# Kernel optimization log

Hardware: AMD Instinct MI355X
Metric: run time of the kernel (lower is better)

The kernel has to match this reference:

```python
import jax, jax.numpy as jnp
import numpy as np

B, H, W, C = 4, 64, 64, 256
D = C // 8  # reduction_ratio = 8


def setup_inputs() -> dict:
    key = jax.random.key(0)
    ks = jax.random.split(key, 6)
    scale = 1.0 / np.sqrt(C)
    return {
        "x": jax.random.normal(ks[0], (B, H, W, C), dtype=jnp.float32),
        "Wf": jax.random.normal(ks[1], (C, D), dtype=jnp.float32) * scale,
        "Wg": jax.random.normal(ks[2], (C, D), dtype=jnp.float32) * scale,
        "Wh": jax.random.normal(ks[3], (C, D), dtype=jnp.float32) * scale,
        "Wv": jax.random.normal(ks[4], (D, C), dtype=jnp.float32) * (1.0 / np.sqrt(D)),
        "gamma": jax.random.normal(ks[5], (), dtype=jnp.float32),
    }


def reference(x, Wf, Wg, Wh, Wv, gamma):
    b, h, w, c = x.shape
    n = h * w
    xf = x.reshape(b, n, c)
    # 1x1 convs (no bias) == per-pixel matmuls over channels
    q = xf @ Wf  # [b, n, d]
    k = xf @ Wg  # [b, n, d]
    v = xf @ Wh  # [b, n, d]
    # beta[i, j] = k_i . q_j ; softmax over last (query) axis, unscaled
    beta = jax.nn.softmax(jnp.einsum('bnd,bmd->bnm', k, q), axis=-1)  # [b, n, n]
    o = jnp.einsum('bnm,bmd->bnd', beta, v)  # [b, n, d]
    o = o.reshape(b, h, w, -1) @ Wv  # output 1x1 conv -> [b, h, w, c]
    return gamma * o + x
```

## Files before the change

### kernel.cpp

```cpp
#include <hip/hip_runtime.h>
#include <hip/hip_bf16.h>
#include <stdint.h>


typedef __attribute__((ext_vector_type(8))) short bf16x8;
typedef __attribute__((ext_vector_type(4))) short bf16x4;
typedef __attribute__((ext_vector_type(8))) _Float16 f16x8;
typedef __attribute__((ext_vector_type(4))) float f32x4;
typedef unsigned short ushort_t;

static __device__ __forceinline__ ushort_t f2bf(float f) {
    __hip_bfloat16 h = __float2bfloat16(f);
    return __builtin_bit_cast(ushort_t, h);
}
static __device__ __forceinline__ float bf2f(ushort_t u) {
    return __bfloat162float(__builtin_bit_cast(__hip_bfloat16, u));
}
static __device__ __forceinline__ ushort_t f2h(float f) {
    _Float16 h = (_Float16)f;
    return __builtin_bit_cast(ushort_t, h);
}
static __device__ __forceinline__ void tsplit(float w, ushort_t& hi, ushort_t& lo) {
    uint32_t b = __builtin_bit_cast(uint32_t, w);
    hi = (ushort_t)(b >> 16);
    float hf = __builtin_bit_cast(float, b & 0xFFFF0000u);
    lo = f2bf(w - hf);
}

static __device__ __forceinline__ f32x4 mfma16bf(bf16x4 a, bf16x4 b, f32x4 c) {
#if __has_builtin(__builtin_amdgcn_mfma_f32_16x16x16bf16_1k)
    return __builtin_amdgcn_mfma_f32_16x16x16bf16_1k(a, b, c, 0, 0, 0);
#else
    f32x4 d;
    asm("v_mfma_f32_16x16x16_bf16 %0, %1, %2, %3"
        : "=v"(d) : "v"(a), "v"(b), "v"(c));
    return d;
#endif
}

static __device__ __forceinline__ float fexp2(float x) {
#if __has_builtin(__builtin_amdgcn_exp2f)
    return __builtin_amdgcn_exp2f(x);
#else
    return exp2f(x);
#endif
}

#define NROWS 16384
#define NTOK  4096
#define QKS   40
#define LOG2E 1.44269504088896340736f

__global__ __launch_bounds__(256) void qkv_kernel(
    const float* __restrict__ x,
    const float* __restrict__ Wf, const float* __restrict__ Wg,
    const float* __restrict__ Wh,
    ushort_t* __restrict__ qh,
    ushort_t* __restrict__ kf,
    ushort_t* __restrict__ vT)
{
    __shared__ __align__(16) ushort_t xh[32 * QKS];
    __shared__ __align__(16) ushort_t xl[32 * QKS];

    const int tid  = threadIdx.x;
    const int wave = tid >> 6;
    const int lane = tid & 63;
    const int ln15 = lane & 15;
    const int quad = lane >> 4;
    const int row0 = blockIdx.x * 32;
    const int rg     = wave & 1;
    const int cgbase = wave >> 1;
    const int r  = tid >> 3;
    const int pp = (tid & 7) * 4;

    f32x4 acc[3];
    #pragma unroll
    for (int ci = 0; ci < 3; ++ci) acc[ci] = (f32x4){0.f, 0.f, 0.f, 0.f};

    float4 xa = *reinterpret_cast<const float4*>(&x[(row0 + r) * 256 + pp]);

    for (int k0 = 0; k0 < 256; k0 += 32) {
        bf16x8 bh[3], bl[3];
        #pragma unroll
        for (int ci = 0; ci < 3; ++ci) {
            int cg = cgbase + ci * 2;
            const float* Wsrc = (cg < 2) ? Wf : (cg < 4) ? Wg : Wh;
            int c = (cg & 1) * 16 + ln15;
            ushort_t hv8[8], lv8[8];
            #pragma unroll
            for (int j = 0; j < 8; ++j) {
                float w = Wsrc[(k0 + quad * 8 + j) * 32 + c];
                tsplit(w, hv8[j], lv8[j]);
            }
            bh[ci] = *reinterpret_cast<bf16x8*>(hv8);
            bl[ci] = *reinterpret_cast<bf16x8*>(lv8);
        }
        float fv[4];
        *reinterpret_cast<float4*>(fv) = xa;
        ushort_t hv[4], lv[4];
        #pragma unroll
        for (int j = 0; j < 4; ++j) tsplit(fv[j], hv[j], lv[j]);
        __syncthreads();
        *reinterpret_cast<uint2*>(&xh[r * QKS + pp]) = *reinterpret_cast<uint2*>(hv);
        *reinterpret_cast<uint2*>(&xl[r * QKS + pp]) = *reinterpret_cast<uint2*>(lv);
        __syncthreads();
        if (k0 < 224)
            xa = *reinterpret_cast<const float4*>(&x[(row0 + r) * 256 + k0 + 32 + pp]);

        const bf16x8 ah = *reinterpret_cast<const bf16x8*>(
            &xh[(rg * 16 + ln15) * QKS + quad * 8]);
        const bf16x8 al = *reinterpret_cast<const bf16x8*>(
            &xl[(rg * 16 + ln15) * QKS + quad * 8]);
        #pragma unroll
        for (int ci = 0; ci < 3; ++ci) {
            acc[ci] = __builtin_amdgcn_mfma_f32_16x16x32_bf16(ah, bh[ci], acc[ci], 0, 0, 0);
            acc[ci] = __builtin_amdgcn_mfma_f32_16x16x32_bf16(al, bh[ci], acc[ci], 0, 0, 0);
            acc[ci] = __builtin_amdgcn_mfma_f32_16x16x32_bf16(ah, bl[ci], acc[ci], 0, 0, 0);
        }
    }

    #pragma unroll
    for (int ci = 0; ci < 3; ++ci) {
        int cg = cgbase + ci * 2;
        int cc = (cg & 1) * 16 + ln15;
        int rowb = row0 + rg * 16 + quad * 4;
        if (cg < 2) {
            #pragma unroll
            for (int rr = 0; rr < 4; ++rr)
                qh[(rowb + rr) * 32 + cc] = f2h(acc[ci][rr] * LOG2E);
        } else if (cg < 4) {
            #pragma unroll
            for (int rr = 0; rr < 4; ++rr)
                kf[(rowb + rr) * 32 + cc] = f2h(acc[ci][rr]);
        } else {
            int bb = row0 >> 12;
            int m  = (row0 & 4095) + rg * 16 + quad * 4;
            ushort4 h4;
            h4.x = f2bf(acc[ci][0]);
            h4.y = f2bf(acc[ci][1]);
            h4.z = f2bf(acc[ci][2]);
            h4.w = f2bf(acc[ci][3]);
            *reinterpret_cast<ushort4*>(&vT[bb * 131072 + cc * 4096 + m]) = h4;
        }
    }
}

__global__ __launch_bounds__(1024, 4) void attn_kernel(
    const ushort_t* __restrict__ qhg,
    const ushort_t* __restrict__ kfg,
    const ushort_t* __restrict__ vT,
    const float* __restrict__ Wv, const float* __restrict__ x,
    const float* __restrict__ gamma, float* __restrict__ out)
{
    __shared__ float Ored[8][32][65];
    __shared__ float Lred[8][64];
    __shared__ float wv[8192];
    __shared__ float Os[64][33];
    __shared__ float linv[64];

    const int tid  = threadIdx.x;
    const int wave = tid >> 6;
    const int lane = tid & 63;
    const int ln15 = lane & 15;
    const int quad = lane >> 4;

    const int b    = blockIdx.x >> 6;
    const int n0   = (blockIdx.x & 63) * 64;
    const int base = b * NTOK;
    const int bb   = b * 131072;

    f16x8 khf[4];
    #pragma unroll
    for (int t = 0; t < 4; ++t)
        khf[t] = *reinterpret_cast<const f16x8*>(
            &kfg[(base + n0 + t * 16 + ln15) * 32 + quad * 8]);

    #pragma unroll
    for (int i = 0; i < 8; ++i) wv[tid + i * 1024] = Wv[tid + i * 1024];

    f32x4 accO[2][4];
    #pragma unroll
    for (int s01 = 0; s01 < 2; ++s01)
        #pragma unroll
        for (int t = 0; t < 4; ++t)
            accO[s01][t] = (f32x4){0.f, 0.f, 0.f, 0.f};
    float lacc[4] = {0.f, 0.f, 0.f, 0.f};

    const int mbase = wave * 16;
    const ushort_t* qp  = qhg + (size_t)(base + mbase + ln15) * 32 + quad * 8;
    const ushort_t* vp0 = vT + bb + ln15 * 4096 + mbase + quad * 4;
    const ushort_t* vp1 = vp0 + 16 * 4096;

    f16x8  qf  = *reinterpret_cast<const f16x8*>(qp);
    bf16x4 va0 = *reinterpret_cast<const bf16x4*>(vp0);
    bf16x4 va1 = *reinterpret_cast<const bf16x4*>(vp1);

    for (int it = 0; it < 16; ++it) {
        qp  += 256 * 32;
        vp0 += 256;
        vp1 += 256;
        f16x8  nqf  = *reinterpret_cast<const f16x8*>(qp);
        bf16x4 nva0 = *reinterpret_cast<const bf16x4*>(vp0);
        bf16x4 nva1 = *reinterpret_cast<const bf16x4*>(vp1);

        #pragma unroll
        for (int t = 0; t < 4; ++t) {
            f32x4 s = __builtin_amdgcn_mfma_f32_16x16x32_f16(
                qf, khf[t], (f32x4){0.f, 0.f, 0.f, 0.f}, 0, 0, 0);

            float p0 = fexp2(s[0]);
            float p1 = fexp2(s[1]);
            float p2 = fexp2(s[2]);
            float p3 = fexp2(s[3]);
            lacc[t] += (p0 + p1) + (p2 + p3);

            ushort_t pu[4];
            pu[0] = f2bf(p0);
            pu[1] = f2bf(p1);
            pu[2] = f2bf(p2);
            pu[3] = f2bf(p3);
            const bf16x4 pb = *reinterpret_cast<bf16x4*>(pu);

            accO[0][t] = mfma16bf(va0, pb, accO[0][t]);
            accO[1][t] = mfma16bf(va1, pb, accO[1][t]);
        }
        qf = nqf; va0 = nva0; va1 = nva1;
    }

    float lr[4];
    #pragma unroll
    for (int t = 0; t < 4; ++t) {
        float v = lacc[t];
        v += __shfl_xor(v, 16);
        v += __shfl_xor(v, 32);
        lr[t] = v;
    }
    if (wave < 8) {
        #pragma unroll
        for (int s01 = 0; s01 < 2; ++s01)
            #pragma unroll
            for (int t = 0; t < 4; ++t)
                #pragma unroll
                for (int rr = 0; rr < 4; ++rr)
                    Ored[wave][s01 * 16 + quad * 4 + rr][t * 16 + ln15] = accO[s01][t][rr];
        if (quad == 0) {
            #pragma unroll
            for (int t = 0; t < 4; ++t) Lred[wave][t * 16 + ln15] = lr[t];
        }
    }
    __syncthreads();
    if (wave >= 8) {
        const int ws = wave - 8;
        #pragma unroll
        for (int s01 = 0; s01 < 2; ++s01)
            #pragma unroll
            for (int t = 0; t < 4; ++t)
                #pragma unroll
                for (int rr = 0; rr < 4; ++rr)
                    Ored[ws][s01 * 16 + quad * 4 + rr][t * 16 + ln15] += accO[s01][t][rr];
        if (quad == 0) {
            #pragma unroll
            for (int t = 0; t < 4; ++t) Lred[ws][t * 16 + ln15] += lr[t];
        }
    }
    __syncthreads();

    #pragma unroll
    for (int i = 0; i < 2; ++i) {
        int idx = i * 1024 + tid;
        int d = idx & 31;
        int n = idx >> 5;
        float v = (Ored[0][d][n] + Ored[1][d][n]) + (Ored[2][d][n] + Ored[3][d][n])
                + (Ored[4][d][n] + Ored[5][d][n]) + (Ored[6][d][n] + Ored[7][d][n]);
        Os[n][d] = v;
    }
    if (tid < 64) {
        float s = (Lred[0][tid] + Lred[1][tid]) + (Lred[2][tid] + Lred[3][tid])
                + (Lred[4][tid] + Lred[5][tid]) + (Lred[6][tid] + Lred[7][tid]);
        linv[tid] = 1.0f / s;
    }
    __syncthreads();

    const float g  = gamma[0];
    const int   c  = tid & 255;
    const int   nh = (tid >> 8) * 16;
    const int rowb = base + n0 + nh;
    #pragma unroll
    for (int rc = 0; rc < 16; rc += 8) {
        float acc[8];
        #pragma unroll
        for (int rr = 0; rr < 8; ++rr) acc[rr] = 0.f;
        for (int d = 0; d < 32; ++d) {
            float wvd = wv[d * 256 + c];
            #pragma unroll
            for (int rr = 0; rr < 8; ++rr) acc[rr] += Os[nh + rc + rr][d] * wvd;
        }
        #pragma unroll
        for (int rr = 0; rr < 8; ++rr) {
            int row = rowb + rc + rr;
            out[row * 256 + c] = g * acc[rr] * linv[nh + rc + rr] + x[row * 256 + c];
        }
    }
}

extern "C" void kernel_launch(void* const* d_in, const int* in_sizes, int n_in,
                              void* d_out, int out_size, void* d_ws, size_t ws_size,
                              hipStream_t stream)
{
    const float* x     = (const float*)d_in[0];
    const float* Wf    = (const float*)d_in[1];
    const float* Wg    = (const float*)d_in[2];
    const float* Wh    = (const float*)d_in[3];
    const float* Wv    = (const float*)d_in[4];
    const float* gamma = (const float*)d_in[5];
    float* out = (float*)d_out;

    ushort_t* qh = (ushort_t*)d_ws;
    ushort_t* kf = qh + NROWS * 32;
    ushort_t* vT = kf + NROWS * 32;

    qkv_kernel<<<dim3(512), dim3(256), 0, stream>>>(x, Wf, Wg, Wh, qh, kf, vT);
    attn_kernel<<<dim3(256), dim3(1024), 0, stream>>>(qh, kf, vT, Wv, x, gamma, out);
}
```

Baseline: 112.8 us.

## Fuse QKV projection and attention into one cooperative kernel with grid sync

Merges the QKV projection kernel and the attention kernel into a single cooperative launch of 256 blocks of 1024 threads. Each block first computes 64 rows of Q/K/V, with the work re-split across 16 waves, then does a grid-wide sync before the attention phase. The Wv shared-memory load is moved ahead of the projection phase. This removes one kernel launch and its gap between kernels, at the cost of a grid barrier, a projection phase in which only half the threads load x, and reliance on all 256 blocks being co-resident.

```diff
diff --git a/kernel.cpp b/kernel.cpp
--- a/kernel.cpp
+++ b/kernel.cpp
@@ -1,7 +1,10 @@
 #include <hip/hip_runtime.h>
 #include <hip/hip_bf16.h>
+#include <hip/hip_cooperative_groups.h>
 #include <stdint.h>
 
+
+namespace cg = cooperative_groups;
 
 typedef __attribute__((ext_vector_type(8))) short bf16x8;
 typedef __attribute__((ext_vector_type(4))) short bf16x4;
@@ -51,118 +54,125 @@
 #define QKS   40
 #define LOG2E 1.44269504088896340736f
 
-__global__ __launch_bounds__(256) void qkv_kernel(
+__global__ __launch_bounds__(1024, 4) void fused_kernel(
     const float* __restrict__ x,
     const float* __restrict__ Wf, const float* __restrict__ Wg,
-    const float* __restrict__ Wh,
-    ushort_t* __restrict__ qh,
-    ushort_t* __restrict__ kf,
+    const float* __restrict__ Wh, const float* __restrict__ Wv,
+    const float* __restrict__ gamma, float* __restrict__ out,
+    ushort_t* __restrict__ qhg,
+    ushort_t* __restrict__ kfg,
     ushort_t* __restrict__ vT)
 {
-    __shared__ __align__(16) ushort_t xh[32 * QKS];
-    __shared__ __align__(16) ushort_t xl[32 * QKS];
+    __shared__ __align__(16) ushort_t xh[64 * QKS];
+    __shared__ __align__(16) ushort_t xl[64 * QKS];
+    __shared__ float Ored[8][32][65];
+    __shared__ float Lred[8][64];
+    __shared__ float wv[8192];
+    __shared__ float Os[64][33];
+    __shared__ float linv[64];
 
     const int tid  = threadIdx.x;
     const int wave = tid >> 6;
     const int lane = tid & 63;
     const int ln15 = lane & 15;
     const int quad = lane >> 4;
-    const int row0 = blockIdx.x * 32;
-    const int rg     = wave & 1;
-    const int cgbase = wave >> 1;
-    const int r  = tid >> 3;
-    const int pp = (tid & 7) * 4;
-
-    f32x4 acc[3];
-    #pragma unroll
-    for (int ci = 0; ci < 3; ++ci) acc[ci] = (f32x4){0.f, 0.f, 0.f, 0.f};
-
-    float4 xa = *reinterpret_cast<const float4*>(&x[(row0 + r) * 256 + pp]);
-
-    for (int k0 = 0; k0 < 256; k0 += 32) {
-        bf16x8 bh[3], bl[3];
-        #pragma unroll
-        for (int ci = 0; ci < 3; ++ci) {
-            int cg = cgbase + ci * 2;
-            const float* Wsrc = (cg < 2) ? Wf : (cg < 4) ? Wg : Wh;
-            int c = (cg & 1) * 16 + ln15;
-            ushort_t hv8[8], lv8[8];
-            #pragma unroll
-            for (int j = 0; j < 8; ++j) {
-                float w = Wsrc[(k0 + quad * 8 + j) * 32 + c];
-                tsplit(w, hv8[j], lv8[j]);
+
+    #pragma unroll
+    for (int i = 0; i < 8; ++i) wv[tid + i * 1024] = Wv[tid + i * 1024];
+
+    {
+        const int row0 = blockIdx.x * 64;
+        const int rg   = wave & 3;
+        const int cg0  = wave >> 2;
+        const int ncg  = (wave < 8) ? 2 : 1;
+        const int r  = tid >> 3;
+        const int pp = (tid & 7) * 4;
+
+        f32x4 acc[2];
+        acc[0] = (f32x4){0.f, 0.f, 0.f, 0.f};
+        acc[1] = (f32x4){0.f, 0.f, 0.f, 0.f};
+
+        float4 xa;
+        if (tid < 512)
+            xa = *reinterpret_cast<const float4*>(&x[(row0 + r) * 256 + pp]);
+
+        for (int k0 = 0; k0 < 256; k0 += 32) {
+            bf16x8 bh[2], bl[2];
+            #pragma unroll
+            for (int ci = 0; ci < 2; ++ci) {
+                if (ci < ncg) {
+                    int cg = cg0 + ci * 4;
+                    const float* Wsrc = (cg < 2) ? Wf : (cg < 4) ? Wg : Wh;
+                    int c = (cg & 1) * 16 + ln15;
+                    ushort_t hv8[8], lv8[8];
+                    #pragma unroll
+                    for (int j = 0; j < 8; ++j) {
+                        float w = Wsrc[(k0 + quad * 8 + j) * 32 + c];
+                        tsplit(w, hv8[j], lv8[j]);
+                    }
+                    bh[ci] = *reinterpret_cast<bf16x8*>(hv8);
+                    bl[ci] = *reinterpret_cast<bf16x8*>(lv8);
+                }
             }
-            bh[ci] = *reinterpret_cast<bf16x8*>(hv8);
-            bl[ci] = *reinterpret_cast<bf16x8*>(lv8);
-        }
-        float fv[4];
-        *reinterpret_cast<float4*>(fv) = xa;
-        ushort_t hv[4], lv[4];
-        #pragma unroll
-        for (int j = 0; j < 4; ++j) tsplit(fv[j], hv[j], lv[j]);
-        __syncthreads();
-        *reinterpret_cast<uint2*>(&xh[r * QKS + pp]) = *reinterpret_cast<uint2*>(hv);
-        *reinterpret_cast<uint2*>(&xl[r * QKS + pp]) = *reinterpret_cast<uint2*>(lv);
-        __syncthreads();
-        if (k0 < 224)
-            xa = *reinterpret_cast<const float4*>(&x[(row0 + r) * 256 + k0 + 32 + pp]);
-
-        const bf16x8 ah = *reinterpret_cast<const bf16x8*>(
-            &xh[(rg * 16 + ln15) * QKS + quad * 8]);
-        const bf16x8 al = *reinterpret_cast<const bf16x8*>(
-            &xl[(rg * 16 + ln15) * QKS + quad * 8]);
-        #pragma unroll
-        for (int ci = 0; ci < 3; ++ci) {
-            acc[ci] = __builtin_amdgcn_mfma_f32_16x16x32_bf16(ah, bh[ci], acc[ci], 0, 0, 0);
-            acc[ci] = __builtin_amdgcn_mfma_f32_16x16x32_bf16(al, bh[ci], acc[ci], 0, 0, 0);
-            acc[ci] = __builtin_amdgcn_mfma_f32_16x16x32_bf16(ah, bl[ci], acc[ci], 0, 0, 0);
-        }
-    }
-
-    #pragma unroll
-    for (int ci = 0; ci < 3; ++ci) {
-        int cg = cgbase + ci * 2;
-        int cc = (cg & 1) * 16 + ln15;
-        int rowb = row0 + rg * 16 + quad * 4;
-        if (cg < 2) {
-            #pragma unroll
-            for (int rr = 0; rr < 4; ++rr)
-                qh[(rowb + rr) * 32 + cc] = f2h(acc[ci][rr] * LOG2E);
-        } else if (cg < 4) {
-            #pragma unroll
-            for (int rr = 0; rr < 4; ++rr)
-                kf[(rowb + rr) * 32 + cc] = f2h(acc[ci][rr]);
-        } else {
-            int bb = row0 >> 12;
-            int m  = (row0 & 4095) + rg * 16 + quad * 4;
-            ushort4 h4;
-            h4.x = f2bf(acc[ci][0]);
-            h4.y = f2bf(acc[ci][1]);
-            h4.z = f2bf(acc[ci][2]);
-            h4.w = f2bf(acc[ci][3]);
-            *reinterpret_cast<ushort4*>(&vT[bb * 131072 + cc * 4096 + m]) = h4;
-        }
-    }
-}
-
-__global__ __launch_bounds__(1024, 4) void attn_kernel(
-    const ushort_t* __restrict__ qhg,
-    const ushort_t* __restrict__ kfg,
-    const ushort_t* __restrict__ vT,
-    const float* __restrict__ Wv, const float* __restrict__ x,
-    const float* __restrict__ gamma, float* __restrict__ out)
-{
-    __shared__ float Ored[8][32][65];
-    __shared__ float Lred[8][64];
-    __shared__ float wv[8192];
-    __shared__ float Os[64][33];
-    __shared__ float linv[64];
-
-    const int tid  = threadIdx.x;
-    const int wave = tid >> 6;
-    const int lane = tid & 63;
-    const int ln15 = lane & 15;
-    const int quad = lane >> 4;
+            __syncthreads();
+            if (tid < 512) {
+                float fv[4];
+                *reinterpret_cast<float4*>(fv) = xa;
+                ushort_t hv[4], lv[4];
+                #pragma unroll
+                for (int j = 0; j < 4; ++j) tsplit(fv[j], hv[j], lv[j]);
+                *reinterpret_cast<uint2*>(&xh[r * QKS + pp]) = *reinterpret_cast<uint2*>(hv);
+                *reinterpret_cast<uint2*>(&xl[r * QKS + pp]) = *reinterpret_cast<uint2*>(lv);
+            }
+            __syncthreads();
+            if (tid < 512 && k0 < 224)
+                xa = *reinterpret_cast<const float4*>(&x[(row0 + r) * 256 + k0 + 32 + pp]);
+
+            const bf16x8 ah = *reinterpret_cast<const bf16x8*>(
+                &xh[(rg * 16 + ln15) * QKS + quad * 8]);
+            const bf16x8 al = *reinterpret_cast<const bf16x8*>(
+                &xl[(rg * 16 + ln15) * QKS + quad * 8]);
+            #pragma unroll
+            for (int ci = 0; ci < 2; ++ci) {
+                if (ci < ncg) {
+                    acc[ci] = __builtin_amdgcn_mfma_f32_16x16x32_bf16(ah, bh[ci], acc[ci], 0, 0, 0);
+                    acc[ci] = __builtin_amdgcn_mfma_f32_16x16x32_bf16(al, bh[ci], acc[ci], 0, 0, 0);
+                    acc[ci] = __builtin_amdgcn_mfma_f32_16x16x32_bf16(ah, bl[ci], acc[ci], 0, 0, 0);
+                }
+            }
+        }
+
+        #pragma unroll
+        for (int ci = 0; ci < 2; ++ci) {
+            if (ci < ncg) {
+                int cg = cg0 + ci * 4;
+                int cc = (cg & 1) * 16 + ln15;
+                int rowb = row0 + rg * 16 + quad * 4;
+                if (cg < 2) {
+                    #pragma unroll
+                    for (int rr = 0; rr < 4; ++rr)
+                        qhg[(rowb + rr) * 32 + cc] = f2h(acc[ci][rr] * LOG2E);
+                } else if (cg < 4) {
+                    #pragma unroll
+                    for (int rr = 0; rr < 4; ++rr)
+                        kfg[(rowb + rr) * 32 + cc] = f2h(acc[ci][rr]);
+                } else {
+                    int bb = row0 >> 12;
+                    int m  = rowb & 4095;
+                    ushort4 h4;
+                    h4.x = f2bf(acc[ci][0]);
+                    h4.y = f2bf(acc[ci][1]);
+                    h4.z = f2bf(acc[ci][2]);
+                    h4.w = f2bf(acc[ci][3]);
+                    *reinterpret_cast<ushort4*>(&vT[bb * 131072 + cc * 4096 + m]) = h4;
+                }
+            }
+        }
+    }
+
+    __threadfence();
+    cg::this_grid().sync();
+    __threadfence();
 
     const int b    = blockIdx.x >> 6;
     const int n0   = (blockIdx.x & 63) * 64;
@@ -174,9 +184,6 @@
     for (int t = 0; t < 4; ++t)
         khf[t] = *reinterpret_cast<const f16x8*>(
             &kfg[(base + n0 + t * 16 + ln15) * 32 + quad * 8]);
-
-    #pragma unroll
-    for (int i = 0; i < 8; ++i) wv[tid + i * 1024] = Wv[tid + i * 1024];
 
     f32x4 accO[2][4];
     #pragma unroll
@@ -319,6 +326,10 @@
     ushort_t* kf = qh + NROWS * 32;
     ushort_t* vT = kf + NROWS * 32;
 
-    qkv_kernel<<<dim3(512), dim3(256), 0, stream>>>(x, Wf, Wg, Wh, qh, kf, vT);
-    attn_kernel<<<dim3(256), dim3(1024), 0, stream>>>(qh, kf, vT, Wv, x, gamma, out);
-}
+    void* args[] = {
+        (void*)&x, (void*)&Wf, (void*)&Wg, (void*)&Wh, (void*)&Wv,
+        (void*)&gamma, (void*)&out, (void*)&qh, (void*)&kf, (void*)&vT
+    };
+    hipLaunchCooperativeKernel((const void*)fused_kernel,
+                               dim3(256), dim3(1024), args, 0, stream);
+}
```

New measurement: 327.9 us. +190.7%, slower.
